# Kernel optimization log

Measured on AMD Instinct MI355X. Metric: run time of the kernel, lower is better.

The kernel has to match this reference:

```python
import jax, jax.numpy as jnp
import numpy as np

S = 8192      # sequence length
E = 1024      # embeddingDimension
D = 64        # linearDimension


def setup_inputs() -> dict:
    key = jax.random.key(0)
    ks = jax.random.split(key, 9)
    lim = 1.0 / np.sqrt(E)
    inp = {
        "x": jax.random.normal(ks[0], (S, E), dtype=jnp.float32),
        "y": jax.random.normal(ks[1], (S, E), dtype=jnp.float32),
        "z": jax.random.normal(ks[2], (S, E), dtype=jnp.float32),
        "Wq": jax.random.uniform(ks[3], (E, D), jnp.float32, -lim, lim),
        "bq": jax.random.uniform(ks[4], (D,), jnp.float32, -lim, lim),
        "Wk": jax.random.uniform(ks[5], (E, D), jnp.float32, -lim, lim),
        "bk": jax.random.uniform(ks[6], (D,), jnp.float32, -lim, lim),
        "Wv": jax.random.uniform(ks[7], (E, D), jnp.float32, -lim, lim),
        "bv": jax.random.uniform(ks[8], (D,), jnp.float32, -lim, lim),
    }
    return inp


def reference(x, y, z, Wq, bq, Wk, bk, Wv, bv):
    q = x @ Wq + bq                      # [S, D]
    k = y @ Wk + bk                      # [S, D]
    v = z @ Wv + bv                      # [S, D]
    scores = q @ k.T                     # [S, S]
    n = scores.shape[0]
    # masked=True: add triu(-inf, diag=1) causal mask (faithful to torch.triu of a full -inf matrix)
    neg_inf = jnp.float32(-jnp.inf)
    causal = jnp.triu(jnp.full((n, n), neg_inf, dtype=scores.dtype), k=1)
    scores = scores + causal
    # original scales by sqrt(size(0)) = sqrt(seq_len), softmax over last dim (torch 2D default)
    attn = jax.nn.softmax(scores / jnp.sqrt(jnp.float32(n)), axis=-1)
    return attn @ v                      # [S, D]
```

## Files before the change

### kernel.cpp

```cpp
#include <hip/hip_runtime.h>

#define SEQ 8192
#define EMB 1024
#define DIM 64

typedef __attribute__((ext_vector_type(8))) short bf16x8;
typedef __attribute__((ext_vector_type(4))) float f32x4;
typedef __attribute__((ext_vector_type(16))) float f32x16;

#if __has_builtin(__builtin_amdgcn_exp2f)
#define EXP2 __builtin_amdgcn_exp2f
#else
#define EXP2 exp2f
#endif

#define SCL 0.0159396779f

__device__ inline unsigned short f2bf(float f) {
    union { float f; unsigned u; } x; x.f = f;
    unsigned r = x.u + 0x7FFFu + ((x.u >> 16) & 1u);
    return (unsigned short)(r >> 16);
}

__device__ inline unsigned cvtpk(float lo, float hi) {
    unsigned r;
    asm("v_cvt_pk_bf16_f32 %0, %1, %2" : "=v"(r) : "v"(lo), "v"(hi));
    return r;
}

__device__ __forceinline__ void gload16(const float* g, float* l) {
    __builtin_amdgcn_global_load_lds(
        (const __attribute__((address_space(1))) unsigned*)g,
        (__attribute__((address_space(3))) unsigned*)l, 16, 0, 0);
}


__global__ __launch_bounds__(256) void wt_kernel(
    const float* __restrict__ Wq, const float* __restrict__ Wk,
    const float* __restrict__ Wv, unsigned short* __restrict__ Wt)
{
    __shared__ float L[64][65];

    const int b   = (int)blockIdx.x;
    const int mat = b >> 4;
    const int kt  = b & 15;
    const float* W = (mat == 0) ? Wq : (mat == 1) ? Wk : Wv;
    const int tid = (int)threadIdx.x;

    const float* src = W + (size_t)kt * 64 * DIM;
    #pragma unroll
    for (int i = 0; i < 16; ++i) {
        const int idx = i * 256 + tid;
        L[idx >> 6][idx & 63] = src[idx];
    }
    __syncthreads();

    unsigned short* dst = Wt + (size_t)(mat * 32 + kt * 2) * 2048;
    #pragma unroll
    for (int h = 0; h < 2; ++h) {
        const int s = tid * 16 + h * 8;
        const int sgo   = s >> 11;
        const int wcg   = (s >> 9) & 3;
        const int lanep = (s >> 3) & 63;
        const int qq = lanep >> 4, c = lanep & 15;
        const int kb = sgo * 32 + qq * 8;
        const int n  = wcg * 16 + c;
        uint4 w4;
        w4.x = cvtpk(L[kb + 0][n], L[kb + 1][n]);
        w4.y = cvtpk(L[kb + 2][n], L[kb + 3][n]);
        w4.z = cvtpk(L[kb + 4][n], L[kb + 5][n]);
        w4.w = cvtpk(L[kb + 6][n], L[kb + 7][n]);
        *(uint4*)&dst[s] = w4;
    }
}

__device__ inline bf16x8 cvt8(float4 a, float4 b) {
    union { unsigned u[4]; bf16x8 v; } r;
    r.u[0] = cvtpk(a.x, a.y);
    r.u[1] = cvtpk(a.z, a.w);
    r.u[2] = cvtpk(b.x, b.y);
    r.u[3] = cvtpk(b.z, b.w);
    return r.v;
}

__global__ __launch_bounds__(512) void proj_kernel(
    const float* __restrict__ x, const float* __restrict__ y, const float* __restrict__ z,
    const float* __restrict__ bq, const float* __restrict__ bk, const float* __restrict__ bv,
    const unsigned short* __restrict__ Wt, unsigned short* __restrict__ qkv)
{
    __shared__ float tile[4][32][128];

    const int bid = (int)blockIdx.x;
    const int mat = bid >> 8;
    const int rb  = (bid & 255) * 32;

    const int tid  = (int)threadIdx.x;
    const int lane = tid & 63;
    const int w    = tid >> 6;
    const int wr   = w >> 2;
    const int wc   = w & 3;
    const int c    = lane & 15;
    const int qq   = lane >> 4;

    const float* X  = (mat == 0) ? x  : (mat == 1) ? y  : z;
    const float* Bv = (mat == 0) ? bq : (mat == 1) ? bk : bv;
    const unsigned short* Wm = Wt + (size_t)mat * 65536;
    unsigned short* outp = qkv + (size_t)mat * (SEQ * DIM);

    f32x4 acc = (f32x4){0.f, 0.f, 0.f, 0.f};

    const int arow = wr * 16 + c;
    const int swl  = arow & 7;
    const unsigned short* Wp = Wm + (size_t)wc * 512 + (size_t)lane * 8;
    const bool swapped = (mat == 1);

    bf16x8 wreg[3][4];

    const int sr0 = w * 4 + (lane >> 5);
    #define STAGE(nb, t)                                                        \
        {                                                                       \
            const int k0_ = (t) * 128;                                          \
            _Pragma("unroll")                                                   \
            for (int j = 0; j < 2; ++j) {                                       \
                const int r_ = sr0 + j * 2;                                     \
                const float* src_ = X + (size_t)(rb + r_) * EMB + k0_           \
                                      + (((lane & 31) ^ (r_ & 7)) << 2);        \
                gload16(src_, &tile[nb][w * 4 + j * 2][0]);                     \
            }                                                                   \
        }

    #define WLOAD(slot, t)                                                      \
        {                                                                       \
            _Pragma("unroll")                                                   \
            for (int s = 0; s < 4; ++s)                                         \
                wreg[slot][s] = *(const bf16x8*)(Wp + (size_t)((t) * 4 + s) * 2048); \
        }

    #define COMP(bt, t)                                                         \
        {                                                                       \
            const float* rowp = &tile[bt][arow][0];                             \
            _Pragma("unroll")                                                   \
            for (int s = 0; s < 4; ++s) {                                       \
                float4 fa = *(const float4*)(rowp + s * 32                      \
                                             + (((qq * 2)     ^ swl) << 2));    \
                float4 fb = *(const float4*)(rowp + s * 32                      \
                                             + (((qq * 2 + 1) ^ swl) << 2));    \
                bf16x8 af = cvt8(fa, fb);                                       \
                bf16x8 bfr = wreg[(t) % 3][s];                                  \
                if (swapped)                                                    \
                    acc = __builtin_amdgcn_mfma_f32_16x16x32_bf16(bfr, af, acc, 0, 0, 0); \
                else                                                            \
                    acc = __builtin_amdgcn_mfma_f32_16x16x32_bf16(af, bfr, acc, 0, 0, 0); \
            }                                                                   \
        }

    STAGE(0, 0);
    WLOAD(0, 0);
    asm volatile("" ::: "memory");
    STAGE(1, 1);
    WLOAD(1, 1);
    asm volatile("" ::: "memory");
    STAGE(2, 2);
    WLOAD(2, 2);

    #pragma unroll
    for (int t = 0; t < 8; ++t) {
        if (t <= 5)      asm volatile("s_waitcnt vmcnt(12)" ::: "memory");
        else if (t == 6) asm volatile("s_waitcnt vmcnt(6)"  ::: "memory");
        else             asm volatile("s_waitcnt vmcnt(0)"  ::: "memory");
        __builtin_amdgcn_s_barrier();
        if (t < 5) STAGE((t + 3) & 3, t + 3);
        COMP(t & 3, t);
        if (t < 5) WLOAD((t + 3) % 3, t + 3);
    }
    #undef STAGE
    #undef WLOAD
    #undef COMP

    const int T = rb >> 5;
    if (mat == 0) {
        const int col = wc * 16 + c;
        const float bb = Bv[col];
        #pragma unroll
        for (int i = 0; i < 4; ++i) {
            const int row = rb + wr * 16 + qq * 4 + i;
            outp[(size_t)row * DIM + col] = f2bf(acc[i] + bb);
        }
    } else if (mat == 1) {
        f32x4 bb4 = *(const f32x4*)&Bv[wc * 16 + qq * 4];
        const int base = (((T * 4 + wc) * 2 + (qq >> 1)) * 32 + wr * 16 + c) * 8 + (qq & 1) * 4;
        uint2 pk;
        pk.x = cvtpk(acc[0] + bb4[0], acc[1] + bb4[1]);
        pk.y = cvtpk(acc[2] + bb4[2], acc[3] + bb4[3]);
        *(uint2*)&outp[base] = pk;
    } else {
        const float bb = Bv[wc * 16 + c];
        const int base = ((((T * 2 + wr) * 2 + (wc >> 1)) * 2 + (qq >> 1)) * 32
                          + (wc & 1) * 16 + c) * 8 + (qq & 1) * 4;
        uint2 pk;
        pk.x = cvtpk(acc[0] + bb, acc[1] + bb);
        pk.y = cvtpk(acc[2] + bb, acc[3] + bb);
        *(uint2*)&outp[base] = pk;
    }
}

__global__ __launch_bounds__(256, 3) void attn_kernel(
    const unsigned short* __restrict__ qkv, float* __restrict__ out,
    float* __restrict__ Opart, float* __restrict__ MLpart)
{
    const unsigned short* Q  = qkv;
    const unsigned short* KF = qkv + SEQ * DIM;
    const unsigned short* VF = qkv + 2 * SEQ * DIM;

    __shared__ float Oall[4][32][68];
    __shared__ float Ml[4][32][2];
    __shared__ float sScl[4][32];
    __shared__ float sM[32];
    __shared__ float sL[32];

    const int u = 1151 - (int)blockIdx.x;
    int g;
    if (u < 32) g = 0; else if (u < 96) g = 1; else if (u < 192) g = 2;
    else if (u < 320) g = 3; else if (u < 480) g = 4; else if (u < 672) g = 5;
    else if (u < 896) g = 6; else g = 7;
    const int o_  = u - 16 * g * (g + 1);
    const int qt  = 32 * g + o_ / (g + 1);
    const int cid = o_ - (o_ / (g + 1)) * (g + 1);

    const int m0 = qt * 32;
    const int tid = (int)threadIdx.x;
    const int lane = tid & 63;
    const int w = tid >> 6;
    const int col = lane & 31;
    const int hi = lane >> 5;

    bf16x8 qf[4];
    {
        const unsigned short* Qr = Q + (size_t)(m0 + col) * DIM + hi * 8;
        #pragma unroll
        for (int ks = 0; ks < 4; ++ks) qf[ks] = *(const bf16x8*)(Qr + ks * 16);
    }

    f32x16 o0, o1;
    #pragma unroll
    for (int r = 0; r < 16; ++r) { o0[r] = 0.f; o1[r] = 0.f; }
    float m_i = -1e30f, l_i = 0.f;

    const int nT = qt + 1;
    const int tb = cid * 32;
    const int te = (tb + 32 < nT) ? (tb + 32) : nT;
    const int nC = te - tb;
    const int w0 = tb + ((nC * w) >> 2);
    const int w1 = tb + ((nC * (w + 1)) >> 2);
    const int nW = w1 - w0;
    const int nP = nW >> 1;

    bf16x8 kA[4], kB[4];
    if (nP > 0) {
        const unsigned short* kb0 = KF + (size_t)w0 * 2048 + (size_t)lane * 8;
        #pragma unroll
        for (int ks = 0; ks < 4; ++ks) kA[ks] = *(const bf16x8*)(kb0 + ks * 512);
        #pragma unroll
        for (int ks = 0; ks < 4; ++ks) kB[ks] = *(const bf16x8*)(kb0 + 2048 + ks * 512);
    }

    for (int pi = 0; pi < nP; ++pi) {
        const int t = w0 + 2 * pi;

        f32x16 sa, sb;
        #pragma unroll
        for (int r = 0; r < 16; ++r) { sa[r] = 0.f; sb[r] = 0.f; }
        __builtin_amdgcn_s_setprio(1);
        #pragma unroll
        for (int ks = 0; ks < 4; ++ks) {
            sa = __builtin_amdgcn_mfma_f32_32x32x16_bf16(kA[ks], qf[ks], sa, 0, 0, 0);
            sb = __builtin_amdgcn_mfma_f32_32x32x16_bf16(kB[ks], qf[ks], sb, 0, 0, 0);
        }
        __builtin_amdgcn_s_setprio(0);

        if (pi + 1 < nP) {
            const unsigned short* kbn = KF + (size_t)(t + 2) * 2048 + (size_t)lane * 8;
            #pragma unroll
            for (int ks = 0; ks < 4; ++ks) kA[ks] = *(const bf16x8*)(kbn + ks * 512);
            #pragma unroll
            for (int ks = 0; ks < 4; ++ks) kB[ks] = *(const bf16x8*)(kbn + 2048 + ks * 512);
        }

        const unsigned short* vb_ = VF + (size_t)t * 2048 + (size_t)lane * 8;
        bf16x8 va[4], vbf[4];
        #pragma unroll
        for (int i = 0; i < 4; ++i) va[i]  = *(const bf16x8*)(vb_ + i * 1024);
        #pragma unroll
        for (int i = 0; i < 4; ++i) vbf[i] = *(const bf16x8*)(vb_ + 512 + i * 1024);

        float p0[16], p1[16];
        #pragma unroll
        for (int r = 0; r < 16; ++r) { p0[r] = sa[r] * SCL; p1[r] = sb[r] * SCL; }
        if (t + 1 == qt) {
            #pragma unroll
            for (int r = 0; r < 16; ++r) {
                const int kvr = (r & 3) + 8 * (r >> 2) + 4 * hi;
                if (kvr > col) p1[r] = -1e30f;
            }
        }
        float tm = fmaxf(p0[0], p1[0]);
        #pragma unroll
        for (int r = 1; r < 16; ++r) tm = fmaxf(tm, fmaxf(p0[r], p1[r]));
        tm = fmaxf(tm, __shfl_xor(tm, 32));
        if (!__all(tm <= m_i + 2.0f)) {
            const float mn = fmaxf(m_i, tm);
            const float alpha = EXP2(m_i - mn);
            m_i = mn;
            l_i *= alpha;
            #pragma unroll
            for (int r = 0; r < 16; ++r) { o0[r] *= alpha; o1[r] *= alpha; }
        }
        float rs = 0.f;
        #pragma unroll
        for (int r = 0; r < 16; ++r) { p0[r] = EXP2(p0[r] - m_i); rs += p0[r]; }
        #pragma unroll
        for (int r = 0; r < 16; ++r) { p1[r] = EXP2(p1[r] - m_i); rs += p1[r]; }
        rs += __shfl_xor(rs, 32);
        l_i += rs;

        unsigned pwA[8], pwB[8];
        #pragma unroll
        for (int i = 0; i < 8; ++i) pwA[i] = cvtpk(p0[2 * i], p0[2 * i + 1]);
        #pragma unroll
        for (int i = 0; i < 8; ++i) pwB[i] = cvtpk(p1[2 * i], p1[2 * i + 1]);
        asm volatile("v_permlane32_swap_b32 %0, %1" : "+v"(pwA[0]), "+v"(pwA[2]));
        asm volatile("v_permlane32_swap_b32 %0, %1" : "+v"(pwA[1]), "+v"(pwA[3]));
        asm volatile("v_permlane32_swap_b32 %0, %1" : "+v"(pwA[4]), "+v"(pwA[6]));
        asm volatile("v_permlane32_swap_b32 %0, %1" : "+v"(pwA[5]), "+v"(pwA[7]));
        asm volatile("v_permlane32_swap_b32 %0, %1" : "+v"(pwB[0]), "+v"(pwB[2]));
        asm volatile("v_permlane32_swap_b32 %0, %1" : "+v"(pwB[1]), "+v"(pwB[3]));
        asm volatile("v_permlane32_swap_b32 %0, %1" : "+v"(pwB[4]), "+v"(pwB[6]));
        asm volatile("v_permlane32_swap_b32 %0, %1" : "+v"(pwB[5]), "+v"(pwB[7]));
        union { unsigned uu[4]; bf16x8 v; } pa0, pa1, pb0, pb1;
        pa0.uu[0] = pwA[0]; pa0.uu[1] = pwA[1]; pa0.uu[2] = pwA[2]; pa0.uu[3] = pwA[3];
        pa1.uu[0] = pwA[4]; pa1.uu[1] = pwA[5]; pa1.uu[2] = pwA[6]; pa1.uu[3] = pwA[7];
        pb0.uu[0] = pwB[0]; pb0.uu[1] = pwB[1]; pb0.uu[2] = pwB[2]; pb0.uu[3] = pwB[3];
        pb1.uu[0] = pwB[4]; pb1.uu[1] = pwB[5]; pb1.uu[2] = pwB[6]; pb1.uu[3] = pwB[7];

        __builtin_amdgcn_s_setprio(1);
        o0 = __builtin_amdgcn_mfma_f32_32x32x16_bf16(va[0],  pa0.v, o0, 0, 0, 0);
        o1 = __builtin_amdgcn_mfma_f32_32x32x16_bf16(vbf[0], pa0.v, o1, 0, 0, 0);
        o0 = __builtin_amdgcn_mfma_f32_32x32x16_bf16(va[1],  pa1.v, o0, 0, 0, 0);
        o1 = __builtin_amdgcn_mfma_f32_32x32x16_bf16(vbf[1], pa1.v, o1, 0, 0, 0);
        o0 = __builtin_amdgcn_mfma_f32_32x32x16_bf16(va[2],  pb0.v, o0, 0, 0, 0);
        o1 = __builtin_amdgcn_mfma_f32_32x32x16_bf16(vbf[2], pb0.v, o1, 0, 0, 0);
        o0 = __builtin_amdgcn_mfma_f32_32x32x16_bf16(va[3],  pb1.v, o0, 0, 0, 0);
        o1 = __builtin_amdgcn_mfma_f32_32x32x16_bf16(vbf[3], pb1.v, o1, 0, 0, 0);
        __builtin_amdgcn_s_setprio(0);
    }

    if (nW & 1) {
        const int t = w1 - 1;
        const unsigned short* kb = KF + (size_t)t * 2048 + (size_t)lane * 8;
        const unsigned short* vb_ = VF + (size_t)t * 2048 + (size_t)lane * 8;
        bf16x8 kT[4];
        #pragma unroll
        for (int ks = 0; ks < 4; ++ks) kT[ks] = *(const bf16x8*)(kb + ks * 512);
        bf16x8 va0 = *(const bf16x8*)(vb_);
        bf16x8 va1 = *(const bf16x8*)(vb_ + 1024);
        bf16x8 vb0 = *(const bf16x8*)(vb_ + 512);
        bf16x8 vb1 = *(const bf16x8*)(vb_ + 1536);

        f32x16 sa;
        #pragma unroll
        for (int r = 0; r < 16; ++r) sa[r] = 0.f;
        __builtin_amdgcn_s_setprio(1);
        #pragma unroll
        for (int ks = 0; ks < 4; ++ks)
            sa = __builtin_amdgcn_mfma_f32_32x32x16_bf16(kT[ks], qf[ks], sa, 0, 0, 0);
        __builtin_amdgcn_s_setprio(0);

        float p0[16];
        #pragma unroll
        for (int r = 0; r < 16; ++r) p0[r] = sa[r] * SCL;
        if (t == qt) {
            #pragma unroll
            for (int r = 0; r < 16; ++r) {
                const int kvr = (r & 3) + 8 * (r >> 2) + 4 * hi;
                if (kvr > col) p0[r] = -1e30f;
            }
        }
        float tm = p0[0];
        #pragma unroll
        for (int r = 1; r < 16; ++r) tm = fmaxf(tm, p0[r]);
        tm = fmaxf(tm, __shfl_xor(tm, 32));
        if (!__all(tm <= m_i + 2.0f)) {
            const float mn = fmaxf(m_i, tm);
            const float alpha = EXP2(m_i - mn);
            m_i = mn;
            l_i *= alpha;
            #pragma unroll
            for (int r = 0; r < 16; ++r) { o0[r] *= alpha; o1[r] *= alpha; }
        }
        float rs = 0.f;
        #pragma unroll
        for (int r = 0; r < 16; ++r) { p0[r] = EXP2(p0[r] - m_i); rs += p0[r]; }
        rs += __shfl_xor(rs, 32);
        l_i += rs;

        unsigned pwA[8];
        #pragma unroll
        for (int i = 0; i < 8; ++i) pwA[i] = cvtpk(p0[2 * i], p0[2 * i + 1]);
        asm volatile("v_permlane32_swap_b32 %0, %1" : "+v"(pwA[0]), "+v"(pwA[2]));
        asm volatile("v_permlane32_swap_b32 %0, %1" : "+v"(pwA[1]), "+v"(pwA[3]));
        asm volatile("v_permlane32_swap_b32 %0, %1" : "+v"(pwA[4]), "+v"(pwA[6]));
        asm volatile("v_permlane32_swap_b32 %0, %1" : "+v"(pwA[5]), "+v"(pwA[7]));
        union { unsigned uu[4]; bf16x8 v; } pa0, pa1;
        pa0.uu[0] = pwA[0]; pa0.uu[1] = pwA[1]; pa0.uu[2] = pwA[2]; pa0.uu[3] = pwA[3];
        pa1.uu[0] = pwA[4]; pa1.uu[1] = pwA[5]; pa1.uu[2] = pwA[6]; pa1.uu[3] = pwA[7];

        __builtin_amdgcn_s_setprio(1);
        o0 = __builtin_amdgcn_mfma_f32_32x32x16_bf16(va0, pa0.v, o0, 0, 0, 0);
        o1 = __builtin_amdgcn_mfma_f32_32x32x16_bf16(vb0, pa0.v, o1, 0, 0, 0);
        o0 = __builtin_amdgcn_mfma_f32_32x32x16_bf16(va1, pa1.v, o0, 0, 0, 0);
        o1 = __builtin_amdgcn_mfma_f32_32x32x16_bf16(vb1, pa1.v, o1, 0, 0, 0);
        __builtin_amdgcn_s_setprio(0);
    }

    #pragma unroll
    for (int r = 0; r < 16; ++r) {
        const int d = (r & 3) + 8 * (r >> 2) + 4 * hi;
        Oall[w][col][d]      = o0[r];
        Oall[w][col][32 + d] = o1[r];
    }
    if (hi == 0) { Ml[w][col][0] = m_i; Ml[w][col][1] = l_i; }
    __syncthreads();

    if (tid < 32) {
        float M = Ml[0][tid][0];
        #pragma unroll
        for (int w2 = 1; w2 < 4; ++w2) M = fmaxf(M, Ml[w2][tid][0]);
        float L = 0.f;
        #pragma unroll
        for (int w2 = 0; w2 < 4; ++w2) {
            const float sc = EXP2(Ml[w2][tid][0] - M);
            sScl[w2][tid] = sc;
            L += Ml[w2][tid][1] * sc;
        }
        sM[tid] = M;
        sL[tid] = L;
    }
    __syncthreads();

    const int r = tid >> 3;
    const int c0 = (tid & 7) * 8;
    f32x4 a0 = (f32x4){0.f, 0.f, 0.f, 0.f};
    f32x4 a1 = (f32x4){0.f, 0.f, 0.f, 0.f};
    #pragma unroll
    for (int w2 = 0; w2 < 4; ++w2) {
        const float sc = sScl[w2][r];
        const float* Orow = &Oall[w2][r][c0];
        a0 += (*(const f32x4*)(Orow)) * sc;
        a1 += (*(const f32x4*)(Orow + 4)) * sc;
    }
    if (qt < 32) {
        const float inv = 1.f / sL[r];
        float* op = out + (size_t)(m0 + r) * DIM + c0;
        *(f32x4*)(op)     = a0 * inv;
        *(f32x4*)(op + 4) = a1 * inv;
    } else {
        const int pb = 16 * (g - 1) * (g + 2) + (qt - 32 * g) * (g + 1) + cid;
        float* op = Opart + (size_t)pb * 2048 + r * 64 + c0;
        *(f32x4*)(op)     = a0;
        *(f32x4*)(op + 4) = a1;
        if (tid < 32) {
            MLpart[(size_t)pb * 64 + tid * 2]     = sM[tid];
            MLpart[(size_t)pb * 64 + tid * 2 + 1] = sL[tid];
        }
    }
}

__global__ __launch_bounds__(256) void fixup_kernel(
    const float* __restrict__ Opart, const float* __restrict__ MLpart,
    float* __restrict__ out)
{
    __shared__ float sScl[8][32];
    __shared__ float sInvL[32];

    const int qt = 32 + (int)blockIdx.x;
    const int g  = qt >> 5;
    const int nc = g + 1;
    const int pb = 16 * (g - 1) * (g + 2) + (qt - 32 * g) * nc;
    const int tid = (int)threadIdx.x;

    if (tid < 32) {
        float M = -1e30f;
        for (int c2 = 0; c2 < nc; ++c2)
            M = fmaxf(M, MLpart[(size_t)(pb + c2) * 64 + tid * 2]);
        float L = 0.f;
        for (int c2 = 0; c2 < nc; ++c2) {
            const float sc = EXP2(MLpart[(size_t)(pb + c2) * 64 + tid * 2] - M);
            sScl[c2][tid] = sc;
            L += MLpart[(size_t)(pb + c2) * 64 + tid * 2 + 1] * sc;
        }
        sInvL[tid] = 1.f / L;
    }
    __syncthreads();

    const int r = tid >> 3;
    const int c0 = (tid & 7) * 8;
    f32x4 a0 = (f32x4){0.f, 0.f, 0.f, 0.f};
    f32x4 a1 = (f32x4){0.f, 0.f, 0.f, 0.f};
    for (int c2 = 0; c2 < nc; ++c2) {
        const float sc = sScl[c2][r];
        const float* Op = Opart + (size_t)(pb + c2) * 2048 + r * 64 + c0;
        a0 += (*(const f32x4*)(Op)) * sc;
        a1 += (*(const f32x4*)(Op + 4)) * sc;
    }
    const float inv = sInvL[r];
    float* op = out + (size_t)(qt * 32 + r) * DIM + c0;
    *(f32x4*)(op)     = a0 * inv;
    *(f32x4*)(op + 4) = a1 * inv;
}

extern "C" void kernel_launch(void* const* d_in, const int* in_sizes, int n_in,
                              void* d_out, int out_size, void* d_ws, size_t ws_size,
                              hipStream_t stream) {
    const float* x  = (const float*)d_in[0];
    const float* y  = (const float*)d_in[1];
    const float* z  = (const float*)d_in[2];
    const float* Wq = (const float*)d_in[3];
    const float* bq = (const float*)d_in[4];
    const float* Wk = (const float*)d_in[5];
    const float* bk = (const float*)d_in[6];
    const float* Wv = (const float*)d_in[7];
    const float* bv = (const float*)d_in[8];

    unsigned short* qkv = (unsigned short*)d_ws;
    unsigned short* Wt  = (unsigned short*)((char*)d_ws + 3145728);
    float* Opart        = (float*)((char*)d_ws + 3538944);
    float* MLpart       = (float*)((char*)d_ws + 12713984);
    float* out          = (float*)d_out;

    hipLaunchKernelGGL(wt_kernel,    dim3(48),   dim3(256), 0, stream, Wq, Wk, Wv, Wt);
    hipLaunchKernelGGL(proj_kernel,  dim3(768),  dim3(512), 0, stream, x, y, z, bq, bk, bv, Wt, qkv);
    hipLaunchKernelGGL(attn_kernel,  dim3(1152), dim3(256), 0, stream, qkv, out, Opart, MLpart);
    hipLaunchKernelGGL(fixup_kernel, dim3(224),  dim3(256), 0, stream, Opart, MLpart, out);
}
```

Measured before the change: 59.45 us.

## Restructure projection kernel to split-K per-wave tiles with LDS reduction

The projection kernel now uses 256 threads, with each wave owning a 16-row by 64-column output tile over half of the K dimension. Each wave stages its own X slice into a private LDS region, which removes the per-iteration block barrier. A final LDS reduction sums the two K halves and writes vectorized 16-byte stores in the layouts the attention kernel expects. This trades fewer waves per block and more weight registers per wave for barrier-free pipelining and wider stores.

```diff
diff --git a/kernel.cpp b/kernel.cpp
--- a/kernel.cpp
+++ b/kernel.cpp
@@ -83,12 +83,12 @@
     return r.v;
 }
 
-__global__ __launch_bounds__(512) void proj_kernel(
+__global__ __launch_bounds__(256) void proj_kernel(
     const float* __restrict__ x, const float* __restrict__ y, const float* __restrict__ z,
     const float* __restrict__ bq, const float* __restrict__ bk, const float* __restrict__ bv,
     const unsigned short* __restrict__ Wt, unsigned short* __restrict__ qkv)
 {
-    __shared__ float tile[4][32][128];
+    __shared__ float pool[12288];
 
     const int bid = (int)blockIdx.x;
     const int mat = bid >> 8;
@@ -97,8 +97,8 @@
     const int tid  = (int)threadIdx.x;
     const int lane = tid & 63;
     const int w    = tid >> 6;
-    const int wr   = w >> 2;
-    const int wc   = w & 3;
+    const int wr   = w & 1;
+    const int kh   = w >> 1;
     const int c    = lane & 15;
     const int qq   = lane >> 4;
 
@@ -107,100 +107,121 @@
     const unsigned short* Wm = Wt + (size_t)mat * 65536;
     unsigned short* outp = qkv + (size_t)mat * (SEQ * DIM);
 
-    f32x4 acc = (f32x4){0.f, 0.f, 0.f, 0.f};
-
-    const int arow = wr * 16 + c;
-    const int swl  = arow & 7;
-    const unsigned short* Wp = Wm + (size_t)wc * 512 + (size_t)lane * 8;
-    const bool swapped = (mat == 1);
-
-    bf16x8 wreg[3][4];
-
-    const int sr0 = w * 4 + (lane >> 5);
-    #define STAGE(nb, t)                                                        \
+    float* poolw = pool + w * 3072;
+    const float* Xw = X + (size_t)(rb + wr * 16) * EMB + kh * 512;
+
+    f32x4 acc[4];
+    #pragma unroll
+    for (int i = 0; i < 4; ++i) acc[i] = (f32x4){0.f, 0.f, 0.f, 0.f};
+
+    bf16x8 wreg[3][8];
+
+    #define STAGE(buf, t)                                                       \
         {                                                                       \
-            const int k0_ = (t) * 128;                                          \
+            const int k0_ = (t) * 64;                                           \
             _Pragma("unroll")                                                   \
-            for (int j = 0; j < 2; ++j) {                                       \
-                const int r_ = sr0 + j * 2;                                     \
-                const float* src_ = X + (size_t)(rb + r_) * EMB + k0_           \
-                                      + (((lane & 31) ^ (r_ & 7)) << 2);        \
-                gload16(src_, &tile[nb][w * 4 + j * 2][0]);                     \
+            for (int j = 0; j < 4; ++j) {                                       \
+                const int rloc = j * 4 + qq;                                    \
+                const int g = c ^ (rloc & 7);                                   \
+                gload16(Xw + (size_t)rloc * EMB + k0_ + g * 4,                  \
+                        poolw + (buf) * 1024 + j * 256);                        \
             }                                                                   \
         }
-
     #define WLOAD(slot, t)                                                      \
         {                                                                       \
+            const int sgb = kh * 16 + (t) * 2;                                  \
             _Pragma("unroll")                                                   \
-            for (int s = 0; s < 4; ++s)                                         \
-                wreg[slot][s] = *(const bf16x8*)(Wp + (size_t)((t) * 4 + s) * 2048); \
-        }
-
-    #define COMP(bt, t)                                                         \
+            for (int ks2 = 0; ks2 < 2; ++ks2)                                   \
+                _Pragma("unroll")                                               \
+                for (int wc2 = 0; wc2 < 4; ++wc2)                               \
+                    wreg[slot][ks2 * 4 + wc2] = *(const bf16x8*)(Wm +           \
+                        ((size_t)((sgb + ks2) * 4 + wc2) * 64 + lane) * 8);     \
+        }
+    #define COMP(bt)                                                            \
         {                                                                       \
-            const float* rowp = &tile[bt][arow][0];                             \
+            const float* rowb = poolw + (bt) * 1024 + c * 64;                   \
             _Pragma("unroll")                                                   \
-            for (int s = 0; s < 4; ++s) {                                       \
-                float4 fa = *(const float4*)(rowp + s * 32                      \
-                                             + (((qq * 2)     ^ swl) << 2));    \
-                float4 fb = *(const float4*)(rowp + s * 32                      \
-                                             + (((qq * 2 + 1) ^ swl) << 2));    \
+            for (int ks2 = 0; ks2 < 2; ++ks2) {                                 \
+                float4 fa = *(const float4*)(rowb +                             \
+                                (((ks2 * 8 + qq * 2)     ^ (c & 7)) << 2));     \
+                float4 fb = *(const float4*)(rowb +                             \
+                                (((ks2 * 8 + qq * 2 + 1) ^ (c & 7)) << 2));     \
                 bf16x8 af = cvt8(fa, fb);                                       \
-                bf16x8 bfr = wreg[(t) % 3][s];                                  \
-                if (swapped)                                                    \
-                    acc = __builtin_amdgcn_mfma_f32_16x16x32_bf16(bfr, af, acc, 0, 0, 0); \
-                else                                                            \
-                    acc = __builtin_amdgcn_mfma_f32_16x16x32_bf16(af, bfr, acc, 0, 0, 0); \
+                _Pragma("unroll")                                               \
+                for (int wc2 = 0; wc2 < 4; ++wc2)                               \
+                    acc[wc2] = __builtin_amdgcn_mfma_f32_16x16x32_bf16(         \
+                        af, wreg[bt][ks2 * 4 + wc2], acc[wc2], 0, 0, 0);        \
             }                                                                   \
         }
 
-    STAGE(0, 0);
-    WLOAD(0, 0);
+    STAGE(0, 0); WLOAD(0, 0);
     asm volatile("" ::: "memory");
-    STAGE(1, 1);
-    WLOAD(1, 1);
+    STAGE(1, 1); WLOAD(1, 1);
     asm volatile("" ::: "memory");
-    STAGE(2, 2);
-    WLOAD(2, 2);
+    STAGE(2, 2); WLOAD(2, 2);
 
     #pragma unroll
     for (int t = 0; t < 8; ++t) {
-        if (t <= 5)      asm volatile("s_waitcnt vmcnt(12)" ::: "memory");
-        else if (t == 6) asm volatile("s_waitcnt vmcnt(6)"  ::: "memory");
+        if (t <= 5)      asm volatile("s_waitcnt vmcnt(24)" ::: "memory");
+        else if (t == 6) asm volatile("s_waitcnt vmcnt(12)" ::: "memory");
         else             asm volatile("s_waitcnt vmcnt(0)"  ::: "memory");
-        __builtin_amdgcn_s_barrier();
-        if (t < 5) STAGE((t + 3) & 3, t + 3);
-        COMP(t & 3, t);
-        if (t < 5) WLOAD((t + 3) % 3, t + 3);
+        COMP(t % 3);
+        if (t < 5) { STAGE(t % 3, t + 3); WLOAD(t % 3, t + 3); }
     }
     #undef STAGE
     #undef WLOAD
     #undef COMP
 
+    __syncthreads();
+    float (*part)[32][68] = (float (*)[32][68])pool;
+    #pragma unroll
+    for (int wc2 = 0; wc2 < 4; ++wc2)
+        #pragma unroll
+        for (int i = 0; i < 4; ++i)
+            part[kh][wr * 16 + qq * 4 + i][wc2 * 16 + c] = acc[wc2][i];
+    __syncthreads();
+
     const int T = rb >> 5;
     if (mat == 0) {
-        const int col = wc * 16 + c;
-        const float bb = Bv[col];
-        #pragma unroll
-        for (int i = 0; i < 4; ++i) {
-            const int row = rb + wr * 16 + qq * 4 + i;
-            outp[(size_t)row * DIM + col] = f2bf(acc[i] + bb);
-        }
+        const int row = tid >> 3;
+        const int c0  = (tid & 7) * 8;
+        float v[8];
+        #pragma unroll
+        for (int j = 0; j < 8; ++j)
+            v[j] = part[0][row][c0 + j] + part[1][row][c0 + j] + Bv[c0 + j];
+        uint4 pk4;
+        pk4.x = cvtpk(v[0], v[1]); pk4.y = cvtpk(v[2], v[3]);
+        pk4.z = cvtpk(v[4], v[5]); pk4.w = cvtpk(v[6], v[7]);
+        *(uint4*)&outp[(size_t)(rb + row) * DIM + c0] = pk4;
     } else if (mat == 1) {
-        f32x4 bb4 = *(const f32x4*)&Bv[wc * 16 + qq * 4];
-        const int base = (((T * 4 + wc) * 2 + (qq >> 1)) * 32 + wr * 16 + c) * 8 + (qq & 1) * 4;
-        uint2 pk;
-        pk.x = cvtpk(acc[0] + bb4[0], acc[1] + bb4[1]);
-        pk.y = cvtpk(acc[2] + bb4[2], acc[3] + bb4[3]);
-        *(uint2*)&outp[base] = pk;
+        const int ks2 = tid >> 6;
+        const int hi2 = (tid >> 5) & 1;
+        const int col = tid & 31;
+        const int d0  = ks2 * 16 + hi2 * 8;
+        float v[8];
+        #pragma unroll
+        for (int j = 0; j < 8; ++j)
+            v[j] = part[0][col][d0 + j] + part[1][col][d0 + j] + Bv[d0 + j];
+        uint4 pk4;
+        pk4.x = cvtpk(v[0], v[1]); pk4.y = cvtpk(v[2], v[3]);
+        pk4.z = cvtpk(v[4], v[5]); pk4.w = cvtpk(v[6], v[7]);
+        *(uint4*)&outp[(size_t)T * 2048 + tid * 8] = pk4;
     } else {
-        const float bb = Bv[wc * 16 + c];
-        const int base = ((((T * 2 + wr) * 2 + (wc >> 1)) * 2 + (qq >> 1)) * 32
-                          + (wc & 1) * 16 + c) * 8 + (qq & 1) * 4;
-        uint2 pk;
-        pk.x = cvtpk(acc[0] + bb, acc[1] + bb);
-        pk.y = cvtpk(acc[2] + bb, acc[3] + bb);
-        *(uint2*)&outp[base] = pk;
+        const int i2  = tid >> 7;
+        const int h   = (tid >> 6) & 1;
+        const int hi2 = (tid >> 5) & 1;
+        const int col = tid & 31;
+        const int r0  = i2 * 16 + hi2 * 8;
+        const int cv  = h * 32 + col;
+        const float bb = Bv[cv];
+        float v[8];
+        #pragma unroll
+        for (int j = 0; j < 8; ++j)
+            v[j] = part[0][r0 + j][cv] + part[1][r0 + j][cv] + bb;
+        uint4 pk4;
+        pk4.x = cvtpk(v[0], v[1]); pk4.y = cvtpk(v[2], v[3]);
+        pk4.z = cvtpk(v[4], v[5]); pk4.w = cvtpk(v[6], v[7]);
+        *(uint4*)&outp[(size_t)T * 2048 + tid * 8] = pk4;
     }
 }
 
@@ -538,7 +559,7 @@
     float* out          = (float*)d_out;
 
     hipLaunchKernelGGL(wt_kernel,    dim3(48),   dim3(256), 0, stream, Wq, Wk, Wv, Wt);
-    hipLaunchKernelGGL(proj_kernel,  dim3(768),  dim3(512), 0, stream, x, y, z, bq, bk, bv, Wt, qkv);
+    hipLaunchKernelGGL(proj_kernel,  dim3(768),  dim3(256), 0, stream, x, y, z, bq, bk, bv, Wt, qkv);
     hipLaunchKernelGGL(attn_kernel,  dim3(1152), dim3(256), 0, stream, qkv, out, Opart, MLpart);
     hipLaunchKernelGGL(fixup_kernel, dim3(224),  dim3(256), 0, stream, Opart, MLpart, out);
 }
```

Measured after the change: 54.40 us. -8.5%, faster.
